# Optimization experiments

Measured on AMD Instinct MI355X. Metric: run time of the kernel, lower is better.

The kernel has to match this reference:

```python
import jax, jax.numpy as jnp
import numpy as np

N_NODES = 100000
N_EDGES = 3200000
N_FEAT = 512
N_GRAPHS = 64
N_EXTRA_LAYERS = 3  # layers 2..4, all 1->1


def setup_inputs() -> dict:
    key = jax.random.key(0)
    ks = jax.random.split(key, 10)
    x = jax.random.normal(ks[0], (N_NODES, N_FEAT), dtype=jnp.float32)
    edge_src = jax.random.randint(ks[1], (N_EDGES,), 0, N_NODES, dtype=jnp.int32)
    edge_dst = jax.random.randint(ks[2], (N_EDGES,), 0, N_NODES, dtype=jnp.int32)
    graph_ids = jnp.sort(jax.random.randint(ks[3], (N_NODES,), 0, N_GRAPHS, dtype=jnp.int32))
    W_neigh0 = jax.random.normal(ks[4], (N_FEAT, 1), dtype=jnp.float32) * 0.05
    W_self0 = jax.random.normal(ks[5], (N_FEAT, 1), dtype=jnp.float32) * 0.05
    b0 = jax.random.normal(ks[6], (1,), dtype=jnp.float32)
    W_neigh_r = jax.random.normal(ks[7], (N_EXTRA_LAYERS, 1, 1), dtype=jnp.float32)
    W_self_r = jax.random.normal(ks[8], (N_EXTRA_LAYERS, 1, 1), dtype=jnp.float32)
    b_r = jax.random.normal(ks[9], (N_EXTRA_LAYERS, 1), dtype=jnp.float32)
    return {"x": x, "edge_src": edge_src, "edge_dst": edge_dst, "graph_ids": graph_ids,
            "W_neigh0": W_neigh0, "W_self0": W_self0, "b0": b0,
            "W_neigh_r": W_neigh_r, "W_self_r": W_self_r, "b_r": b_r}


def _conv_wl(h, edge_src, edge_dst, W_neigh, W_self, b, n_nodes):
    # GraphConv(norm='none'): project first (in >= out here), gather at src, scatter-sum at dst, + bias
    proj = h @ W_neigh                      # [N, out]
    neigh = jax.ops.segment_sum(proj[edge_src], edge_dst, num_segments=n_nodes) + b
    return neigh + h @ W_self               # residual self-loop linear (no bias)


def reference(x, edge_src, edge_dst, graph_ids, W_neigh0, W_self0, b0, W_neigh_r, W_self_r, b_r):
    n = x.shape[0]
    xs = [x]
    h = jax.nn.relu(_conv_wl(x, edge_src, edge_dst, W_neigh0, W_self0, b0, n))
    xs.append(h)
    for i in range(W_neigh_r.shape[0]):
        h = jax.nn.relu(_conv_wl(h, edge_src, edge_dst, W_neigh_r[i], W_self_r[i], b_r[i], n))
        xs.append(h)
    hcat = jnp.concatenate(xs, axis=1)       # [N, F + num_layers] (concat_features=True)
    # dgl.sum_nodes: per-graph sum over the batched graph
    return jax.ops.segment_sum(hcat, graph_ids, num_segments=N_GRAPHS)  # [G, F + L]
```

## Files before the change

kernel.cpp:

```cpp
#include <hip/hip_runtime.h>

#define N_NODES  100000
#define N_EDGES  3200000
#define N_FEAT   512
#define N_GRAPHS 64
#define N_COLS   516
#define NBINS    1563
#define B1       256
#define EPB      (N_EDGES / B1)
#define CHUNK    25
#define NWAVES   (N_NODES / CHUNK)
#define SRC_MASK 0x1FFFF

__global__ __launch_bounds__(1024) void prep_kernel(
    const int* __restrict__ edst, const int* __restrict__ gid,
    int* __restrict__ histG, int* __restrict__ starts, float* __restrict__ outz)
{
    __shared__ int lh[NBINS];
    const int b = blockIdx.x, tid = threadIdx.x;
    const int gtid = b * 1024 + tid;

    if (gtid < N_GRAPHS * N_COLS) outz[gtid] = 0.f;
    if (gtid < N_NODES) {
        const int g = gid[gtid];
        const int gp = gtid ? gid[gtid - 1] : -1;
        for (int q = gp + 1; q <= g; ++q) starts[q] = gtid;
        if (gtid == N_NODES - 1)
            for (int q = g + 1; q <= N_GRAPHS; ++q) starts[q] = N_NODES;
    }
    for (int i = tid; i < NBINS; i += 1024) lh[i] = 0;
    __syncthreads();
    const int e0 = b * EPB;
    for (int e = e0 + tid; e < e0 + EPB; e += 1024)
        atomicAdd(&lh[edst[e] >> 6], 1);
    __syncthreads();
    for (int i = tid; i < NBINS; i += 1024) histG[i * B1 + b] = lh[i];
}

__device__ __forceinline__ void flush_cs(
    int si, int cur_g, const float a[8], int wave, int lane,
    float* __restrict__ pp, int* __restrict__ pt, float* __restrict__ out)
{
    if (si < 2) {
        const int slot = wave * 2 + si;
        if (lane == 0) pt[slot] = cur_g;
        float* d = pp + (size_t)slot * N_FEAT + lane * 8;
        *(float4*)d       = make_float4(a[0], a[1], a[2], a[3]);
        *(float4*)(d + 4) = make_float4(a[4], a[5], a[6], a[7]);
    } else {
        float* o = out + (size_t)cur_g * N_COLS + lane * 8;
        #pragma unroll
        for (int k = 0; k < 8; ++k) atomicAdd(o + k, a[k]);
    }
}

__global__ __launch_bounds__(256) void pass_x_kernel(
    const float* __restrict__ x, const int* __restrict__ gid,
    const float* __restrict__ wn, const float* __restrict__ ws,
    float* __restrict__ p0, float* __restrict__ s0,
    float* __restrict__ neigh, float* __restrict__ out,
    float* __restrict__ pp, int* __restrict__ pt)
{
    const int wave = (blockIdx.x * blockDim.x + threadIdx.x) >> 6;
    const int lane = threadIdx.x & 63;
    const int start = wave * CHUNK, end = start + CHUNK;

    for (int n = start + lane; n < end; n += 64) neigh[n] = 0.f;

    const float4 wna = *(const float4*)(wn + lane * 8);
    const float4 wnb = *(const float4*)(wn + lane * 8 + 4);
    const float4 wsa = *(const float4*)(ws + lane * 8);
    const float4 wsb = *(const float4*)(ws + lane * 8 + 4);

    float a[8] = {0.f, 0.f, 0.f, 0.f, 0.f, 0.f, 0.f, 0.f};
    int cur_g = gid[start];
    const bool uniform = (gid[end - 1] == cur_g);
    int si = 0;

    for (int n = start; n < end; ++n) {
        if (!uniform) {
            const int g = gid[n];
            if (g != cur_g) {
                flush_cs(si, cur_g, a, wave, lane, pp, pt, out);
                ++si;
                #pragma unroll
                for (int k = 0; k < 8; ++k) a[k] = 0.f;
                cur_g = g;
            }
        }
        const float* row = x + (size_t)n * N_FEAT;
        const float4 xa = *(const float4*)(row + lane * 8);
        const float4 xb = *(const float4*)(row + lane * 8 + 4);

        a[0] += xa.x; a[1] += xa.y; a[2] += xa.z; a[3] += xa.w;
        a[4] += xb.x; a[5] += xb.y; a[6] += xb.z; a[7] += xb.w;

        float dn = xa.x*wna.x + xa.y*wna.y + xa.z*wna.z + xa.w*wna.w
                 + xb.x*wnb.x + xb.y*wnb.y + xb.z*wnb.z + xb.w*wnb.w;
        float dv = xa.x*wsa.x + xa.y*wsa.y + xa.z*wsa.z + xa.w*wsa.w
                 + xb.x*wsb.x + xb.y*wsb.y + xb.z*wsb.z + xb.w*wsb.w;
        #pragma unroll
        for (int off = 32; off > 0; off >>= 1) {
            dn += __shfl_down(dn, off);
            dv += __shfl_down(dv, off);
        }
        if (lane == 0) { p0[n] = dn; s0[n] = dv; }
    }
    flush_cs(si, cur_g, a, wave, lane, pp, pt, out);
    ++si;
    if (lane == 0)
        for (int s2 = si; s2 < 2; ++s2) pt[wave * 2 + s2] = -1;
}

__global__ __launch_bounds__(512) void reduce_x_kernel(
    const float* __restrict__ pp, const int* __restrict__ pt,
    const int* __restrict__ starts, float* __restrict__ out)
{
    const int g = blockIdx.x, c = threadIdx.x;
    const int s = starts[g], e = starts[g + 1];
    float acc = 0.f;
    if (e > s) {
        const int w0 = s / CHUNK, w1 = (e - 1) / CHUNK;
        for (int w = w0; w <= w1; ++w) {
            #pragma unroll
            for (int k = 0; k < 2; ++k) {
                const int slot = w * 2 + k;
                if (pt[slot] == g) acc += pp[(size_t)slot * N_FEAT + c];
            }
        }
    }
    out[(size_t)g * N_COLS + c] += acc;
}

__global__ __launch_bounds__(256) void colscan_kernel(
    const int* __restrict__ histG, int* __restrict__ colscanG,
    int* __restrict__ totalG)
{
    __shared__ int sc[256];
    const int bin = blockIdx.x, t = threadIdx.x;
    const int v = histG[bin * B1 + t];
    sc[t] = v;
    __syncthreads();
    for (int off = 1; off < 256; off <<= 1) {
        const int a = (t >= off) ? sc[t - off] : 0;
        __syncthreads();
        sc[t] += a;
        __syncthreads();
    }
    colscanG[bin * B1 + t] = sc[t] - v;
    if (t == 255) totalG[bin] = sc[255];
}

__global__ __launch_bounds__(256) void scan2_kernel(
    const int* __restrict__ totalG, int* __restrict__ binstart)
{
    __shared__ int sc[256];
    const int t = threadIdx.x;
    const int CH = 7;
    int loc[CH];
    int s = 0;
    for (int i = 0; i < CH; ++i) {
        const int bin = t * CH + i;
        const int v = (bin < NBINS) ? totalG[bin] : 0;
        loc[i] = s; s += v;
    }
    const int my = s;
    sc[t] = my;
    __syncthreads();
    for (int off = 1; off < 256; off <<= 1) {
        const int a = (t >= off) ? sc[t - off] : 0;
        __syncthreads();
        sc[t] += a;
        __syncthreads();
    }
    const int texcl = sc[t] - my;
    for (int i = 0; i < CH; ++i) {
        const int bin = t * CH + i;
        if (bin < NBINS) binstart[bin] = texcl + loc[i];
    }
    if (t == 255) binstart[NBINS] = sc[255];
}

__global__ __launch_bounds__(1024) void reorder_kernel(
    const int* __restrict__ esrc, const int* __restrict__ edst,
    const int* __restrict__ binstart, const int* __restrict__ colscanG,
    int* __restrict__ sorted)
{
    __shared__ int offs[NBINS];
    const int b = blockIdx.x, tid = threadIdx.x;
    for (int i = tid; i < NBINS; i += 1024)
        offs[i] = binstart[i] + colscanG[i * B1 + b];
    __syncthreads();
    const int e0 = b * EPB;
    for (int e = e0 + tid; e < e0 + EPB; e += 1024) {
        const int s = esrc[e], d = edst[e];
        const int p = atomicAdd(&offs[d >> 6], 1);
        sorted[p] = s | ((d & 63) << 17);
    }
}

__global__ __launch_bounds__(256) void binned_scatter_kernel(
    const int* __restrict__ sorted, const int* __restrict__ binstart,
    const float* __restrict__ pin, const float* __restrict__ self_in,
    const float* __restrict__ wself_p, const float* __restrict__ bias_p,
    const float* __restrict__ wnext_p,
    float* __restrict__ h_out, float* __restrict__ p_next,
    const int* __restrict__ gid, float* __restrict__ out, int col)
{
    __shared__ float acc[4][64];
    const int b = blockIdx.x, tid = threadIdx.x;
    ((float*)acc)[tid] = 0.f;
    __syncthreads();

    const int st = binstart[b], en = binstart[b + 1];
    const int w = tid >> 6;
    for (int e = st + tid; e < en; e += 256) {
        const int v = sorted[e];
        atomicAdd(&acc[w][v >> 17], pin[v & SRC_MASK]);
    }
    __syncthreads();

    if (tid < 64) {
        const int n = b * 64 + tid;
        const bool valid = (n < N_NODES);
        float h = 0.f;
        int g = 0;
        if (valid) {
            const float nb = acc[0][tid] + acc[1][tid] + acc[2][tid] + acc[3][tid];
            const float sw = wself_p ? *wself_p : 1.0f;
            const float v = nb + *bias_p + sw * self_in[n];
            h = v > 0.f ? v : 0.f;
            h_out[n] = h;
            if (wnext_p) p_next[n] = h * (*wnext_p);
            g = gid[n];
        }
        const int g0 = __shfl(g, 0);
        if (__all(!valid || g == g0)) {
            float s = h;
            #pragma unroll
            for (int off = 32; off > 0; off >>= 1) s += __shfl_down(s, off);
            if (tid == 0) atomicAdd(&out[(size_t)g0 * N_COLS + col], s);
        } else if (valid) {
            atomicAdd(&out[(size_t)g * N_COLS + col], h);
        }
    }
}

extern "C" void kernel_launch(void* const* d_in, const int* in_sizes, int n_in,
                              void* d_out, int out_size, void* d_ws, size_t ws_size,
                              hipStream_t stream)
{
    (void)in_sizes; (void)n_in; (void)out_size; (void)ws_size;

    const float* x    = (const float*)d_in[0];
    const int*   esrc = (const int*)d_in[1];
    const int*   edst = (const int*)d_in[2];
    const int*   gid  = (const int*)d_in[3];
    const float* Wn0  = (const float*)d_in[4];
    const float* Ws0  = (const float*)d_in[5];
    const float* b0p  = (const float*)d_in[6];
    const float* Wnr  = (const float*)d_in[7];
    const float* Wsr  = (const float*)d_in[8];
    const float* brp  = (const float*)d_in[9];
    float* out = (float*)d_out;

    float* pp    = (float*)d_ws;
    float* bufP  = pp + (size_t)NWAVES * 2 * N_FEAT;
    float* bufP2 = bufP  + N_NODES;
    float* bufS  = bufP2 + N_NODES;
    float* bufH  = bufS  + N_NODES;
    int*   pt       = (int*)(bufH + N_NODES);
    int*   starts   = pt + NWAVES * 2;
    int*   binstart = starts + (N_GRAPHS + 1);
    int*   totalG   = binstart + NBINS + 1;
    int*   histG    = totalG + NBINS;
    int*   colscanG = histG + (size_t)NBINS * B1;
    int*   sorted   = colscanG + (size_t)NBINS * B1;

    prep_kernel<<<B1, 1024, 0, stream>>>(edst, gid, histG, starts, out);
    pass_x_kernel<<<NWAVES / 4, 256, 0, stream>>>(
        x, gid, Wn0, Ws0, bufP, bufS, bufP2 ,
        out, pp, pt);
    colscan_kernel<<<NBINS, 256, 0, stream>>>(histG, colscanG, totalG);
    scan2_kernel<<<1, 256, 0, stream>>>(totalG, binstart);
    reorder_kernel<<<B1, 1024, 0, stream>>>(esrc, edst, binstart, colscanG, sorted);
    reduce_x_kernel<<<N_GRAPHS, 512, 0, stream>>>(pp, pt, starts, out);

    binned_scatter_kernel<<<NBINS, 256, 0, stream>>>(
        sorted, binstart, bufP, bufS, nullptr, b0p, Wnr + 0, bufH, bufP2, gid, out, 512);
    binned_scatter_kernel<<<NBINS, 256, 0, stream>>>(
        sorted, binstart, bufP2, bufH, Wsr + 0, brp + 0, Wnr + 1, bufH, bufP, gid, out, 513);
    binned_scatter_kernel<<<NBINS, 256, 0, stream>>>(
        sorted, binstart, bufP, bufH, Wsr + 1, brp + 1, Wnr + 2, bufH, bufP2, gid, out, 514);
    binned_scatter_kernel<<<NBINS, 256, 0, stream>>>(
        sorted, binstart, bufP2, bufH, Wsr + 2, brp + 2, nullptr, bufH, nullptr, gid, out, 515);
}
```

Before: 509.8 us.

## Merge preprocessing and layer kernels into two cooperative grid-synced kernels

Replaces the ten separate kernel launches with two cooperative kernels. One handles histogram, column scan, the x pass, the bin prefix scan and the edge reorder, separated by grid.sync. The other runs the per-graph x reduction and all four scatter layers in a persistent 1024-block grid. The column scan now uses wave shuffles instead of a shared-memory block scan. This removes launch gaps between stages, but cooperative launches cap the grid at what can be co-resident, which limits parallelism, and grid.sync carries its own cost. The x pass now overlaps the column scan in one phase, and the x reduction overlaps the first layer.

```diff
diff --git a/kernel.cpp b/kernel.cpp
--- a/kernel.cpp
+++ b/kernel.cpp
@@ -1,4 +1,7 @@
 #include <hip/hip_runtime.h>
+#include <hip/hip_cooperative_groups.h>
+
+namespace cg = cooperative_groups;
 
 #define N_NODES  100000
 #define N_EDGES  3200000
@@ -11,31 +14,7 @@
 #define CHUNK    25
 #define NWAVES   (N_NODES / CHUNK)
 #define SRC_MASK 0x1FFFF
-
-__global__ __launch_bounds__(1024) void prep_kernel(
-    const int* __restrict__ edst, const int* __restrict__ gid,
-    int* __restrict__ histG, int* __restrict__ starts, float* __restrict__ outz)
-{
-    __shared__ int lh[NBINS];
-    const int b = blockIdx.x, tid = threadIdx.x;
-    const int gtid = b * 1024 + tid;
-
-    if (gtid < N_GRAPHS * N_COLS) outz[gtid] = 0.f;
-    if (gtid < N_NODES) {
-        const int g = gid[gtid];
-        const int gp = gtid ? gid[gtid - 1] : -1;
-        for (int q = gp + 1; q <= g; ++q) starts[q] = gtid;
-        if (gtid == N_NODES - 1)
-            for (int q = g + 1; q <= N_GRAPHS; ++q) starts[q] = N_NODES;
-    }
-    for (int i = tid; i < NBINS; i += 1024) lh[i] = 0;
-    __syncthreads();
-    const int e0 = b * EPB;
-    for (int e = e0 + tid; e < e0 + EPB; e += 1024)
-        atomicAdd(&lh[edst[e] >> 6], 1);
-    __syncthreads();
-    for (int i = tid; i < NBINS; i += 1024) histG[i * B1 + b] = lh[i];
-}
+#define GRID_B   1024
 
 __device__ __forceinline__ void flush_cs(
     int si, int cur_g, const float a[8], int wave, int lane,
@@ -54,196 +33,237 @@
     }
 }
 
-__global__ __launch_bounds__(256) void pass_x_kernel(
-    const float* __restrict__ x, const int* __restrict__ gid,
+__global__ __launch_bounds__(1024) void mega_prep_kernel(
+    const float* __restrict__ x, const int* __restrict__ esrc,
+    const int* __restrict__ edst, const int* __restrict__ gid,
     const float* __restrict__ wn, const float* __restrict__ ws,
     float* __restrict__ p0, float* __restrict__ s0,
-    float* __restrict__ neigh, float* __restrict__ out,
-    float* __restrict__ pp, int* __restrict__ pt)
-{
-    const int wave = (blockIdx.x * blockDim.x + threadIdx.x) >> 6;
-    const int lane = threadIdx.x & 63;
-    const int start = wave * CHUNK, end = start + CHUNK;
-
-    for (int n = start + lane; n < end; n += 64) neigh[n] = 0.f;
-
-    const float4 wna = *(const float4*)(wn + lane * 8);
-    const float4 wnb = *(const float4*)(wn + lane * 8 + 4);
-    const float4 wsa = *(const float4*)(ws + lane * 8);
-    const float4 wsb = *(const float4*)(ws + lane * 8 + 4);
-
-    float a[8] = {0.f, 0.f, 0.f, 0.f, 0.f, 0.f, 0.f, 0.f};
-    int cur_g = gid[start];
-    const bool uniform = (gid[end - 1] == cur_g);
-    int si = 0;
-
-    for (int n = start; n < end; ++n) {
-        if (!uniform) {
-            const int g = gid[n];
-            if (g != cur_g) {
-                flush_cs(si, cur_g, a, wave, lane, pp, pt, out);
-                ++si;
-                #pragma unroll
-                for (int k = 0; k < 8; ++k) a[k] = 0.f;
-                cur_g = g;
-            }
-        }
-        const float* row = x + (size_t)n * N_FEAT;
-        const float4 xa = *(const float4*)(row + lane * 8);
-        const float4 xb = *(const float4*)(row + lane * 8 + 4);
-
-        a[0] += xa.x; a[1] += xa.y; a[2] += xa.z; a[3] += xa.w;
-        a[4] += xb.x; a[5] += xb.y; a[6] += xb.z; a[7] += xb.w;
-
-        float dn = xa.x*wna.x + xa.y*wna.y + xa.z*wna.z + xa.w*wna.w
-                 + xb.x*wnb.x + xb.y*wnb.y + xb.z*wnb.z + xb.w*wnb.w;
-        float dv = xa.x*wsa.x + xa.y*wsa.y + xa.z*wsa.z + xa.w*wsa.w
-                 + xb.x*wsb.x + xb.y*wsb.y + xb.z*wsb.z + xb.w*wsb.w;
-        #pragma unroll
-        for (int off = 32; off > 0; off >>= 1) {
-            dn += __shfl_down(dn, off);
-            dv += __shfl_down(dv, off);
-        }
-        if (lane == 0) { p0[n] = dn; s0[n] = dv; }
-    }
-    flush_cs(si, cur_g, a, wave, lane, pp, pt, out);
-    ++si;
-    if (lane == 0)
-        for (int s2 = si; s2 < 2; ++s2) pt[wave * 2 + s2] = -1;
-}
-
-__global__ __launch_bounds__(512) void reduce_x_kernel(
-    const float* __restrict__ pp, const int* __restrict__ pt,
-    const int* __restrict__ starts, float* __restrict__ out)
-{
-    const int g = blockIdx.x, c = threadIdx.x;
-    const int s = starts[g], e = starts[g + 1];
-    float acc = 0.f;
-    if (e > s) {
-        const int w0 = s / CHUNK, w1 = (e - 1) / CHUNK;
-        for (int w = w0; w <= w1; ++w) {
+    float* __restrict__ out, float* __restrict__ pp, int* __restrict__ pt,
+    int* __restrict__ histG, int* __restrict__ colscanG, int* __restrict__ totalG,
+    int* __restrict__ starts, int* __restrict__ binstart, int* __restrict__ sorted)
+{
+    __shared__ int lh[NBINS];
+    cg::grid_group grid = cg::this_grid();
+    const int b = blockIdx.x, tid = threadIdx.x;
+    const int gtid = b * 1024 + tid;
+
+    if (gtid < N_GRAPHS * N_COLS) out[gtid] = 0.f;
+    if (gtid < N_NODES) {
+        const int g = gid[gtid];
+        const int gp = gtid ? gid[gtid - 1] : -1;
+        for (int q = gp + 1; q <= g; ++q) starts[q] = gtid;
+        if (gtid == N_NODES - 1)
+            for (int q = g + 1; q <= N_GRAPHS; ++q) starts[q] = N_NODES;
+    }
+    for (int i = tid; i < NBINS; i += 1024) lh[i] = 0;
+    __syncthreads();
+    {
+        const int e0 = b * EPB;
+        for (int e = e0 + tid; e < e0 + EPB; e += 1024)
+            atomicAdd(&lh[edst[e] >> 6], 1);
+    }
+    __syncthreads();
+    for (int i = tid; i < NBINS; i += 1024) histG[i * B1 + b] = lh[i];
+
+    grid.sync();
+
+    const int gwave = gtid >> 6;
+    const int lane = tid & 63;
+
+    if (gwave < NBINS) {
+        const int4 v = *(const int4*)(histG + (size_t)gwave * B1 + lane * 4);
+        const int s1 = v.x, s2 = s1 + v.y, s3 = s2 + v.z;
+        const int tot = s3 + v.w;
+        int incl = tot;
+        #pragma unroll
+        for (int off = 1; off < 64; off <<= 1) {
+            const int t = __shfl_up(incl, off);
+            if (lane >= off) incl += t;
+        }
+        const int excl = incl - tot;
+        *(int4*)(colscanG + (size_t)gwave * B1 + lane * 4) =
+            make_int4(excl, excl + s1, excl + s2, excl + s3);
+        if (lane == 63) totalG[gwave] = incl;
+    }
+
+    if (gwave < NWAVES) {
+        const int start = gwave * CHUNK, end = start + CHUNK;
+
+        const float4 wna = *(const float4*)(wn + lane * 8);
+        const float4 wnb = *(const float4*)(wn + lane * 8 + 4);
+        const float4 wsa = *(const float4*)(ws + lane * 8);
+        const float4 wsb = *(const float4*)(ws + lane * 8 + 4);
+
+        float a[8] = {0.f, 0.f, 0.f, 0.f, 0.f, 0.f, 0.f, 0.f};
+        int cur_g = gid[start];
+        const bool uniform = (gid[end - 1] == cur_g);
+        int si = 0;
+
+        for (int n = start; n < end; ++n) {
+            if (!uniform) {
+                const int g = gid[n];
+                if (g != cur_g) {
+                    flush_cs(si, cur_g, a, gwave, lane, pp, pt, out);
+                    ++si;
+                    #pragma unroll
+                    for (int k = 0; k < 8; ++k) a[k] = 0.f;
+                    cur_g = g;
+                }
+            }
+            const float* row = x + (size_t)n * N_FEAT;
+            const float4 xa = *(const float4*)(row + lane * 8);
+            const float4 xb = *(const float4*)(row + lane * 8 + 4);
+
+            a[0] += xa.x; a[1] += xa.y; a[2] += xa.z; a[3] += xa.w;
+            a[4] += xb.x; a[5] += xb.y; a[6] += xb.z; a[7] += xb.w;
+
+            float dn = xa.x*wna.x + xa.y*wna.y + xa.z*wna.z + xa.w*wna.w
+                     + xb.x*wnb.x + xb.y*wnb.y + xb.z*wnb.z + xb.w*wnb.w;
+            float dv = xa.x*wsa.x + xa.y*wsa.y + xa.z*wsa.z + xa.w*wsa.w
+                     + xb.x*wsb.x + xb.y*wsb.y + xb.z*wsb.z + xb.w*wsb.w;
             #pragma unroll
-            for (int k = 0; k < 2; ++k) {
-                const int slot = w * 2 + k;
-                if (pt[slot] == g) acc += pp[(size_t)slot * N_FEAT + c];
-            }
-        }
-    }
-    out[(size_t)g * N_COLS + c] += acc;
-}
-
-__global__ __launch_bounds__(256) void colscan_kernel(
-    const int* __restrict__ histG, int* __restrict__ colscanG,
-    int* __restrict__ totalG)
-{
-    __shared__ int sc[256];
-    const int bin = blockIdx.x, t = threadIdx.x;
-    const int v = histG[bin * B1 + t];
-    sc[t] = v;
+            for (int off = 32; off > 0; off >>= 1) {
+                dn += __shfl_down(dn, off);
+                dv += __shfl_down(dv, off);
+            }
+            if (lane == 0) { p0[n] = dn; s0[n] = dv; }
+        }
+        flush_cs(si, cur_g, a, gwave, lane, pp, pt, out);
+        ++si;
+        if (lane == 0)
+            for (int s2i = si; s2i < 2; ++s2i) pt[gwave * 2 + s2i] = -1;
+    }
+
+    grid.sync();
+
+    if (b == 0 && tid < 64) {
+        int loc[25];
+        int s = 0;
+        #pragma unroll
+        for (int i = 0; i < 25; ++i) {
+            const int bin = tid * 25 + i;
+            loc[i] = s;
+            s += (bin < NBINS) ? totalG[bin] : 0;
+        }
+        int incl = s;
+        #pragma unroll
+        for (int off = 1; off < 64; off <<= 1) {
+            const int t = __shfl_up(incl, off);
+            if (tid >= off) incl += t;
+        }
+        const int excl = incl - s;
+        #pragma unroll
+        for (int i = 0; i < 25; ++i) {
+            const int bin = tid * 25 + i;
+            if (bin <= NBINS) binstart[bin] = excl + loc[i];
+        }
+    }
+
+    grid.sync();
+
+    for (int i = tid; i < NBINS; i += 1024)
+        lh[i] = binstart[i] + colscanG[i * B1 + b];
     __syncthreads();
-    for (int off = 1; off < 256; off <<= 1) {
-        const int a = (t >= off) ? sc[t - off] : 0;
-        __syncthreads();
-        sc[t] += a;
-        __syncthreads();
-    }
-    colscanG[bin * B1 + t] = sc[t] - v;
-    if (t == 255) totalG[bin] = sc[255];
-}
-
-__global__ __launch_bounds__(256) void scan2_kernel(
-    const int* __restrict__ totalG, int* __restrict__ binstart)
-{
-    __shared__ int sc[256];
-    const int t = threadIdx.x;
-    const int CH = 7;
-    int loc[CH];
-    int s = 0;
-    for (int i = 0; i < CH; ++i) {
-        const int bin = t * CH + i;
-        const int v = (bin < NBINS) ? totalG[bin] : 0;
-        loc[i] = s; s += v;
-    }
-    const int my = s;
-    sc[t] = my;
-    __syncthreads();
-    for (int off = 1; off < 256; off <<= 1) {
-        const int a = (t >= off) ? sc[t - off] : 0;
-        __syncthreads();
-        sc[t] += a;
-        __syncthreads();
-    }
-    const int texcl = sc[t] - my;
-    for (int i = 0; i < CH; ++i) {
-        const int bin = t * CH + i;
-        if (bin < NBINS) binstart[bin] = texcl + loc[i];
-    }
-    if (t == 255) binstart[NBINS] = sc[255];
-}
-
-__global__ __launch_bounds__(1024) void reorder_kernel(
-    const int* __restrict__ esrc, const int* __restrict__ edst,
-    const int* __restrict__ binstart, const int* __restrict__ colscanG,
-    int* __restrict__ sorted)
-{
-    __shared__ int offs[NBINS];
-    const int b = blockIdx.x, tid = threadIdx.x;
-    for (int i = tid; i < NBINS; i += 1024)
-        offs[i] = binstart[i] + colscanG[i * B1 + b];
-    __syncthreads();
-    const int e0 = b * EPB;
-    for (int e = e0 + tid; e < e0 + EPB; e += 1024) {
-        const int s = esrc[e], d = edst[e];
-        const int p = atomicAdd(&offs[d >> 6], 1);
-        sorted[p] = s | ((d & 63) << 17);
-    }
-}
-
-__global__ __launch_bounds__(256) void binned_scatter_kernel(
+    {
+        const int e0 = b * EPB;
+        for (int e = e0 + tid; e < e0 + EPB; e += 1024) {
+            const int s = esrc[e], d = edst[e];
+            const int p = atomicAdd(&lh[d >> 6], 1);
+            sorted[p] = s | ((d & 63) << 17);
+        }
+    }
+}
+
+__device__ __forceinline__ void scatter_layer(
     const int* __restrict__ sorted, const int* __restrict__ binstart,
     const float* __restrict__ pin, const float* __restrict__ self_in,
     const float* __restrict__ wself_p, const float* __restrict__ bias_p,
     const float* __restrict__ wnext_p,
     float* __restrict__ h_out, float* __restrict__ p_next,
-    const int* __restrict__ gid, float* __restrict__ out, int col)
+    const int* __restrict__ gid, float* __restrict__ out, int col,
+    float (*acc)[64])
+{
+    const int tid = threadIdx.x;
+    const float sw    = wself_p ? *wself_p : 1.0f;
+    const float bias  = *bias_p;
+    const float wnext = wnext_p ? *wnext_p : 0.0f;
+
+    for (int b = blockIdx.x; b < NBINS; b += GRID_B) {
+        ((float*)acc)[tid] = 0.f;
+        __syncthreads();
+        const int st = binstart[b], en = binstart[b + 1];
+        const int w = tid >> 6;
+        for (int e = st + tid; e < en; e += 256) {
+            const int v = sorted[e];
+            atomicAdd(&acc[w][v >> 17], pin[v & SRC_MASK]);
+        }
+        __syncthreads();
+        if (tid < 64) {
+            const int n = b * 64 + tid;
+            const bool valid = (n < N_NODES);
+            float h = 0.f;
+            int g = 0;
+            if (valid) {
+                const float nb = acc[0][tid] + acc[1][tid] + acc[2][tid] + acc[3][tid];
+                const float v = nb + bias + sw * self_in[n];
+                h = v > 0.f ? v : 0.f;
+                h_out[n] = h;
+                if (wnext_p) p_next[n] = h * wnext;
+                g = gid[n];
+            }
+            const int g0 = __shfl(g, 0);
+            if (__all(!valid || g == g0)) {
+                float sacc = h;
+                #pragma unroll
+                for (int off = 32; off > 0; off >>= 1) sacc += __shfl_down(sacc, off);
+                if (tid == 0) atomicAdd(&out[(size_t)g0 * N_COLS + col], sacc);
+            } else if (valid) {
+                atomicAdd(&out[(size_t)g * N_COLS + col], h);
+            }
+        }
+        __syncthreads();
+    }
+}
+
+__global__ __launch_bounds__(256) void layers_kernel(
+    const int* __restrict__ sorted, const int* __restrict__ binstart,
+    const int* __restrict__ gid, float* __restrict__ out,
+    float* __restrict__ bufP, float* __restrict__ bufS,
+    float* __restrict__ bufP2, float* __restrict__ bufH,
+    const float* __restrict__ b0p, const float* __restrict__ Wnr,
+    const float* __restrict__ Wsr, const float* __restrict__ brp,
+    const float* __restrict__ pp, const int* __restrict__ pt,
+    const int* __restrict__ starts)
 {
     __shared__ float acc[4][64];
-    const int b = blockIdx.x, tid = threadIdx.x;
-    ((float*)acc)[tid] = 0.f;
-    __syncthreads();
-
-    const int st = binstart[b], en = binstart[b + 1];
-    const int w = tid >> 6;
-    for (int e = st + tid; e < en; e += 256) {
-        const int v = sorted[e];
-        atomicAdd(&acc[w][v >> 17], pin[v & SRC_MASK]);
-    }
-    __syncthreads();
-
-    if (tid < 64) {
-        const int n = b * 64 + tid;
-        const bool valid = (n < N_NODES);
-        float h = 0.f;
-        int g = 0;
-        if (valid) {
-            const float nb = acc[0][tid] + acc[1][tid] + acc[2][tid] + acc[3][tid];
-            const float sw = wself_p ? *wself_p : 1.0f;
-            const float v = nb + *bias_p + sw * self_in[n];
-            h = v > 0.f ? v : 0.f;
-            h_out[n] = h;
-            if (wnext_p) p_next[n] = h * (*wnext_p);
-            g = gid[n];
-        }
-        const int g0 = __shfl(g, 0);
-        if (__all(!valid || g == g0)) {
-            float s = h;
-            #pragma unroll
-            for (int off = 32; off > 0; off >>= 1) s += __shfl_down(s, off);
-            if (tid == 0) atomicAdd(&out[(size_t)g0 * N_COLS + col], s);
-        } else if (valid) {
-            atomicAdd(&out[(size_t)g * N_COLS + col], h);
-        }
-    }
+    cg::grid_group grid = cg::this_grid();
+
+    if (blockIdx.x >= GRID_B - N_GRAPHS) {
+        const int g = blockIdx.x - (GRID_B - N_GRAPHS);
+        const int s = starts[g], e = starts[g + 1];
+        for (int c = threadIdx.x; c < N_FEAT; c += 256) {
+            float accv = 0.f;
+            if (e > s) {
+                const int w0 = s / CHUNK, w1 = (e - 1) / CHUNK;
+                for (int w = w0; w <= w1; ++w) {
+                    #pragma unroll
+                    for (int k = 0; k < 2; ++k) {
+                        const int slot = w * 2 + k;
+                        if (pt[slot] == g) accv += pp[(size_t)slot * N_FEAT + c];
+                    }
+                }
+            }
+            out[(size_t)g * N_COLS + c] += accv;
+        }
+    }
+
+    scatter_layer(sorted, binstart, bufP,  bufS, nullptr, b0p,     Wnr + 0, bufH, bufP2, gid, out, 512, acc);
+    grid.sync();
+    scatter_layer(sorted, binstart, bufP2, bufH, Wsr + 0, brp + 0, Wnr + 1, bufH, bufP,  gid, out, 513, acc);
+    grid.sync();
+    scatter_layer(sorted, binstart, bufP,  bufH, Wsr + 1, brp + 1, Wnr + 2, bufH, bufP2, gid, out, 514, acc);
+    grid.sync();
+    scatter_layer(sorted, binstart, bufP2, bufH, Wsr + 2, brp + 2, nullptr, bufH, nullptr, gid, out, 515, acc);
 }
 
 extern "C" void kernel_launch(void* const* d_in, const int* in_sizes, int n_in,
@@ -271,27 +291,31 @@
     float* bufH  = bufS  + N_NODES;
     int*   pt       = (int*)(bufH + N_NODES);
     int*   starts   = pt + NWAVES * 2;
-    int*   binstart = starts + (N_GRAPHS + 1);
-    int*   totalG   = binstart + NBINS + 1;
-    int*   histG    = totalG + NBINS;
+    int*   binstart = starts + 68;
+    int*   totalG   = binstart + 1564;
+    int*   histG    = totalG + 1564;
     int*   colscanG = histG + (size_t)NBINS * B1;
     int*   sorted   = colscanG + (size_t)NBINS * B1;
 
-    prep_kernel<<<B1, 1024, 0, stream>>>(edst, gid, histG, starts, out);
-    pass_x_kernel<<<NWAVES / 4, 256, 0, stream>>>(
-        x, gid, Wn0, Ws0, bufP, bufS, bufP2 ,
-        out, pp, pt);
-    colscan_kernel<<<NBINS, 256, 0, stream>>>(histG, colscanG, totalG);
-    scan2_kernel<<<1, 256, 0, stream>>>(totalG, binstart);
-    reorder_kernel<<<B1, 1024, 0, stream>>>(esrc, edst, binstart, colscanG, sorted);
-    reduce_x_kernel<<<N_GRAPHS, 512, 0, stream>>>(pp, pt, starts, out);
-
-    binned_scatter_kernel<<<NBINS, 256, 0, stream>>>(
-        sorted, binstart, bufP, bufS, nullptr, b0p, Wnr + 0, bufH, bufP2, gid, out, 512);
-    binned_scatter_kernel<<<NBINS, 256, 0, stream>>>(
-        sorted, binstart, bufP2, bufH, Wsr + 0, brp + 0, Wnr + 1, bufH, bufP, gid, out, 513);
-    binned_scatter_kernel<<<NBINS, 256, 0, stream>>>(
-        sorted, binstart, bufP, bufH, Wsr + 1, brp + 1, Wnr + 2, bufH, bufP2, gid, out, 514);
-    binned_scatter_kernel<<<NBINS, 256, 0, stream>>>(
-        sorted, binstart, bufP2, bufH, Wsr + 2, brp + 2, nullptr, bufH, nullptr, gid, out, 515);
-}
+    {
+        void* args[] = {
+            (void*)&x, (void*)&esrc, (void*)&edst, (void*)&gid,
+            (void*)&Wn0, (void*)&Ws0, (void*)&bufP, (void*)&bufS,
+            (void*)&out, (void*)&pp, (void*)&pt,
+            (void*)&histG, (void*)&colscanG, (void*)&totalG,
+            (void*)&starts, (void*)&binstart, (void*)&sorted
+        };
+        hipLaunchCooperativeKernel((const void*)mega_prep_kernel,
+                                   dim3(B1), dim3(1024), args, 0, stream);
+    }
+    {
+        void* args[] = {
+            (void*)&sorted, (void*)&binstart, (void*)&gid, (void*)&out,
+            (void*)&bufP, (void*)&bufS, (void*)&bufP2, (void*)&bufH,
+            (void*)&b0p, (void*)&Wnr, (void*)&Wsr, (void*)&brp,
+            (void*)&pp, (void*)&pt, (void*)&starts
+        };
+        hipLaunchCooperativeKernel((const void*)layers_kernel,
+                                   dim3(GRID_B), dim3(256), args, 0, stream);
+    }
+}
```

After: 1.022 ms. 101% more time.

## Bin edges by source and push-scatter with global atomics instead of pull-gather

Applied to the files above, without the earlier changes.

Edges are now binned by source node rather than destination. Each block computes the previous layer's activation for its 64 source nodes into shared memory, then atomically adds into a global per-layer neighbour buffer indexed by destination, and a new final kernel finishes the last layer. This swaps random global gathers of the projection for random global float atomics. It also adds four zeroed neighbour buffers and one extra kernel launch.

```diff
diff --git a/kernel.cpp b/kernel.cpp
--- a/kernel.cpp
+++ b/kernel.cpp
@@ -6,21 +6,24 @@
 #define N_GRAPHS 64
 #define N_COLS   516
 #define NBINS    1563
+#define NEIGH_PAD 100032
 #define B1       256
 #define EPB      (N_EDGES / B1)
 #define CHUNK    25
 #define NWAVES   (N_NODES / CHUNK)
-#define SRC_MASK 0x1FFFF
+#define DST_MASK 0x1FFFF
 
 __global__ __launch_bounds__(1024) void prep_kernel(
-    const int* __restrict__ edst, const int* __restrict__ gid,
-    int* __restrict__ histG, int* __restrict__ starts, float* __restrict__ outz)
+    const int* __restrict__ esrc, const int* __restrict__ gid,
+    int* __restrict__ histG, int* __restrict__ starts,
+    float* __restrict__ outz, float* __restrict__ neigh)
 {
     __shared__ int lh[NBINS];
     const int b = blockIdx.x, tid = threadIdx.x;
     const int gtid = b * 1024 + tid;
 
     if (gtid < N_GRAPHS * N_COLS) outz[gtid] = 0.f;
+    for (int i = gtid; i < 4 * NEIGH_PAD; i += B1 * 1024) neigh[i] = 0.f;
     if (gtid < N_NODES) {
         const int g = gid[gtid];
         const int gp = gtid ? gid[gtid - 1] : -1;
@@ -32,7 +35,7 @@
     __syncthreads();
     const int e0 = b * EPB;
     for (int e = e0 + tid; e < e0 + EPB; e += 1024)
-        atomicAdd(&lh[edst[e] >> 6], 1);
+        atomicAdd(&lh[esrc[e] >> 6], 1);
     __syncthreads();
     for (int i = tid; i < NBINS; i += 1024) histG[i * B1 + b] = lh[i];
 }
@@ -58,14 +61,12 @@
     const float* __restrict__ x, const int* __restrict__ gid,
     const float* __restrict__ wn, const float* __restrict__ ws,
     float* __restrict__ p0, float* __restrict__ s0,
-    float* __restrict__ neigh, float* __restrict__ out,
+    float* __restrict__ out,
     float* __restrict__ pp, int* __restrict__ pt)
 {
     const int wave = (blockIdx.x * blockDim.x + threadIdx.x) >> 6;
     const int lane = threadIdx.x & 63;
     const int start = wave * CHUNK, end = start + CHUNK;
-
-    for (int n = start + lane; n < end; n += 64) neigh[n] = 0.f;
 
     const float4 wna = *(const float4*)(wn + lane * 8);
     const float4 wnb = *(const float4*)(wn + lane * 8 + 4);
@@ -194,55 +195,87 @@
     const int e0 = b * EPB;
     for (int e = e0 + tid; e < e0 + EPB; e += 1024) {
         const int s = esrc[e], d = edst[e];
-        const int p = atomicAdd(&offs[d >> 6], 1);
-        sorted[p] = s | ((d & 63) << 17);
-    }
-}
-
-__global__ __launch_bounds__(256) void binned_scatter_kernel(
+        const int p = atomicAdd(&offs[s >> 6], 1);
+        sorted[p] = d | ((s & 63) << 17);
+    }
+}
+
+__global__ __launch_bounds__(256) void scatter_kernel(
     const int* __restrict__ sorted, const int* __restrict__ binstart,
-    const float* __restrict__ pin, const float* __restrict__ self_in,
-    const float* __restrict__ wself_p, const float* __restrict__ bias_p,
+    const float* __restrict__ neigh_in,
+    const float* __restrict__ p_in,
+    const float* __restrict__ self_in,
+    const float* __restrict__ wself_p,
+    const float* __restrict__ bias_p,
     const float* __restrict__ wnext_p,
-    float* __restrict__ h_out, float* __restrict__ p_next,
-    const int* __restrict__ gid, float* __restrict__ out, int col)
-{
-    __shared__ float acc[4][64];
+    float* __restrict__ h_out,
+    const int* __restrict__ gid, float* __restrict__ out, int col,
+    float* __restrict__ neigh_out)
+{
+    __shared__ float ps[64];
     const int b = blockIdx.x, tid = threadIdx.x;
-    ((float*)acc)[tid] = 0.f;
-    __syncthreads();
-
-    const int st = binstart[b], en = binstart[b + 1];
-    const int w = tid >> 6;
-    for (int e = st + tid; e < en; e += 256) {
-        const int v = sorted[e];
-        atomicAdd(&acc[w][v >> 17], pin[v & SRC_MASK]);
-    }
-    __syncthreads();
 
     if (tid < 64) {
         const int n = b * 64 + tid;
         const bool valid = (n < N_NODES);
-        float h = 0.f;
-        int g = 0;
-        if (valid) {
-            const float nb = acc[0][tid] + acc[1][tid] + acc[2][tid] + acc[3][tid];
-            const float sw = wself_p ? *wself_p : 1.0f;
-            const float v = nb + *bias_p + sw * self_in[n];
-            h = v > 0.f ? v : 0.f;
-            h_out[n] = h;
-            if (wnext_p) p_next[n] = h * (*wnext_p);
-            g = gid[n];
+        float p = 0.f;
+        if (neigh_in) {
+            float h = 0.f;
+            int g = 0;
+            if (valid) {
+                const float sw = wself_p ? *wself_p : 1.0f;
+                const float v = neigh_in[n] + *bias_p + sw * self_in[n];
+                h = v > 0.f ? v : 0.f;
+                h_out[n] = h;
+                g = gid[n];
+            }
+            p = h * (*wnext_p);
+            const int g0 = __shfl(g, 0);
+            if (__all(!valid || g == g0)) {
+                float s = h;
+                #pragma unroll
+                for (int off = 32; off > 0; off >>= 1) s += __shfl_down(s, off);
+                if (tid == 0) atomicAdd(&out[(size_t)g0 * N_COLS + col], s);
+            } else if (valid) {
+                atomicAdd(&out[(size_t)g * N_COLS + col], h);
+            }
+        } else {
+            if (valid) p = p_in[n];
         }
-        const int g0 = __shfl(g, 0);
-        if (__all(!valid || g == g0)) {
-            float s = h;
-            #pragma unroll
-            for (int off = 32; off > 0; off >>= 1) s += __shfl_down(s, off);
-            if (tid == 0) atomicAdd(&out[(size_t)g0 * N_COLS + col], s);
-        } else if (valid) {
-            atomicAdd(&out[(size_t)g * N_COLS + col], h);
-        }
+        ps[tid] = p;
+    }
+    __syncthreads();
+
+    const int st = binstart[b], en = binstart[b + 1];
+    for (int e = st + tid; e < en; e += 256) {
+        const int v = sorted[e];
+        atomicAdd(&neigh_out[v & DST_MASK], ps[v >> 17]);
+    }
+}
+
+__global__ __launch_bounds__(64) void final_kernel(
+    const float* __restrict__ neigh_in, const float* __restrict__ h_prev,
+    const float* __restrict__ wself_p, const float* __restrict__ bias_p,
+    const int* __restrict__ gid, float* __restrict__ out)
+{
+    const int b = blockIdx.x, tid = threadIdx.x;
+    const int n = b * 64 + tid;
+    const bool valid = (n < N_NODES);
+    float h = 0.f;
+    int g = 0;
+    if (valid) {
+        const float v = neigh_in[n] + *bias_p + (*wself_p) * h_prev[n];
+        h = v > 0.f ? v : 0.f;
+        g = gid[n];
+    }
+    const int g0 = __shfl(g, 0);
+    if (__all(!valid || g == g0)) {
+        float s = h;
+        #pragma unroll
+        for (int off = 32; off > 0; off >>= 1) s += __shfl_down(s, off);
+        if (tid == 0) atomicAdd(&out[(size_t)g0 * N_COLS + 515], s);
+    } else if (valid) {
+        atomicAdd(&out[(size_t)g * N_COLS + 515], h);
     }
 }
 
@@ -266,32 +299,40 @@
 
     float* pp    = (float*)d_ws;
     float* bufP  = pp + (size_t)NWAVES * 2 * N_FEAT;
-    float* bufP2 = bufP  + N_NODES;
-    float* bufS  = bufP2 + N_NODES;
-    float* bufH  = bufS  + N_NODES;
-    int*   pt       = (int*)(bufH + N_NODES);
+    float* bufS  = bufP + N_NODES;
+    float* bufH1 = bufS + N_NODES;
+    float* bufH2 = bufH1 + N_NODES;
+    float* bufH3 = bufH2 + N_NODES;
+    float* neigh = bufH3 + N_NODES;
+    float* n0 = neigh,             *n1 = neigh + NEIGH_PAD;
+    float* n2 = neigh + 2*NEIGH_PAD, *n3 = neigh + 3*NEIGH_PAD;
+    int*   pt       = (int*)(neigh + 4 * NEIGH_PAD);
     int*   starts   = pt + NWAVES * 2;
-    int*   binstart = starts + (N_GRAPHS + 1);
-    int*   totalG   = binstart + NBINS + 1;
-    int*   histG    = totalG + NBINS;
+    int*   binstart = starts + 68;
+    int*   totalG   = binstart + 1564;
+    int*   histG    = totalG + 1564;
     int*   colscanG = histG + (size_t)NBINS * B1;
     int*   sorted   = colscanG + (size_t)NBINS * B1;
 
-    prep_kernel<<<B1, 1024, 0, stream>>>(edst, gid, histG, starts, out);
+    prep_kernel<<<B1, 1024, 0, stream>>>(esrc, gid, histG, starts, out, neigh);
     pass_x_kernel<<<NWAVES / 4, 256, 0, stream>>>(
-        x, gid, Wn0, Ws0, bufP, bufS, bufP2 ,
-        out, pp, pt);
+        x, gid, Wn0, Ws0, bufP, bufS, out, pp, pt);
     colscan_kernel<<<NBINS, 256, 0, stream>>>(histG, colscanG, totalG);
     scan2_kernel<<<1, 256, 0, stream>>>(totalG, binstart);
     reorder_kernel<<<B1, 1024, 0, stream>>>(esrc, edst, binstart, colscanG, sorted);
     reduce_x_kernel<<<N_GRAPHS, 512, 0, stream>>>(pp, pt, starts, out);
 
-    binned_scatter_kernel<<<NBINS, 256, 0, stream>>>(
-        sorted, binstart, bufP, bufS, nullptr, b0p, Wnr + 0, bufH, bufP2, gid, out, 512);
-    binned_scatter_kernel<<<NBINS, 256, 0, stream>>>(
-        sorted, binstart, bufP2, bufH, Wsr + 0, brp + 0, Wnr + 1, bufH, bufP, gid, out, 513);
-    binned_scatter_kernel<<<NBINS, 256, 0, stream>>>(
-        sorted, binstart, bufP, bufH, Wsr + 1, brp + 1, Wnr + 2, bufH, bufP2, gid, out, 514);
-    binned_scatter_kernel<<<NBINS, 256, 0, stream>>>(
-        sorted, binstart, bufP2, bufH, Wsr + 2, brp + 2, nullptr, bufH, nullptr, gid, out, 515);
-}
+    scatter_kernel<<<NBINS, 256, 0, stream>>>(
+        sorted, binstart, nullptr, bufP, nullptr, nullptr, nullptr, nullptr,
+        nullptr, gid, out, -1, n0);
+    scatter_kernel<<<NBINS, 256, 0, stream>>>(
+        sorted, binstart, n0, nullptr, bufS, nullptr, b0p, Wnr + 0,
+        bufH1, gid, out, 512, n1);
+    scatter_kernel<<<NBINS, 256, 0, stream>>>(
+        sorted, binstart, n1, nullptr, bufH1, Wsr + 0, brp + 0, Wnr + 1,
+        bufH2, gid, out, 513, n2);
+    scatter_kernel<<<NBINS, 256, 0, stream>>>(
+        sorted, binstart, n2, nullptr, bufH2, Wsr + 1, brp + 1, Wnr + 2,
+        bufH3, gid, out, 514, n3);
+    final_kernel<<<NBINS, 64, 0, stream>>>(n3, bufH3, Wsr + 2, brp + 2, gid, out);
+}
```

After: 1.087 ms. 113% more time.

## Bin edges into 2D src/dst tiles so source values come from LDS

Applied to the files above, without the earlier changes.

Edges are now bucketed by (source chunk of 4096, destination chunk of 8192) instead of by destination only. Each tile block stages its source projections and a destination accumulator in shared memory, so the random gathers move from global memory to LDS. Per-source-chunk partials go to a global buffer, and a new reduce/update kernel sums the 25 partials per node. This adds a partial-buffer round trip and one extra kernel launch per layer. The prep histogram is also replicated eight ways to cut shared-atomic contention.

```diff
diff --git a/kernel.cpp b/kernel.cpp
--- a/kernel.cpp
+++ b/kernel.cpp
@@ -5,18 +5,26 @@
 #define N_FEAT   512
 #define N_GRAPHS 64
 #define N_COLS   516
-#define NBINS    1563
 #define B1       256
 #define EPB      (N_EDGES / B1)
 #define CHUNK    25
 #define NWAVES   (N_NODES / CHUNK)
-#define SRC_MASK 0x1FFFF
+
+#define SC_SHIFT 12
+#define SC       4096
+#define DC_SHIFT 13
+#define DC       8192
+#define NS       25
+#define ND       13
+#define NT       (NS * ND)
+#define NPAD     (ND * DC)
 
 __global__ __launch_bounds__(1024) void prep_kernel(
-    const int* __restrict__ edst, const int* __restrict__ gid,
+    const int* __restrict__ esrc, const int* __restrict__ edst,
+    const int* __restrict__ gid,
     int* __restrict__ histG, int* __restrict__ starts, float* __restrict__ outz)
 {
-    __shared__ int lh[NBINS];
+    __shared__ int lh[8][NT];
     const int b = blockIdx.x, tid = threadIdx.x;
     const int gtid = b * 1024 + tid;
 
@@ -28,13 +36,21 @@
         if (gtid == N_NODES - 1)
             for (int q = g + 1; q <= N_GRAPHS; ++q) starts[q] = N_NODES;
     }
-    for (int i = tid; i < NBINS; i += 1024) lh[i] = 0;
-    __syncthreads();
+    for (int i = tid; i < 8 * NT; i += 1024) ((int*)lh)[i] = 0;
+    __syncthreads();
+    const int r = (tid >> 7) & 7;
     const int e0 = b * EPB;
-    for (int e = e0 + tid; e < e0 + EPB; e += 1024)
-        atomicAdd(&lh[edst[e] >> 6], 1);
-    __syncthreads();
-    for (int i = tid; i < NBINS; i += 1024) histG[i * B1 + b] = lh[i];
+    for (int e = e0 + tid; e < e0 + EPB; e += 1024) {
+        const int t = (esrc[e] >> SC_SHIFT) * ND + (edst[e] >> DC_SHIFT);
+        atomicAdd(&lh[r][t], 1);
+    }
+    __syncthreads();
+    for (int i = tid; i < NT; i += 1024) {
+        int s = 0;
+        s += lh[0][i]; s += lh[1][i]; s += lh[2][i]; s += lh[3][i];
+        s += lh[4][i]; s += lh[5][i]; s += lh[6][i]; s += lh[7][i];
+        histG[i * B1 + b] = s;
+    }
 }
 
 __device__ __forceinline__ void flush_cs(
@@ -58,14 +74,12 @@
     const float* __restrict__ x, const int* __restrict__ gid,
     const float* __restrict__ wn, const float* __restrict__ ws,
     float* __restrict__ p0, float* __restrict__ s0,
-    float* __restrict__ neigh, float* __restrict__ out,
+    float* __restrict__ out,
     float* __restrict__ pp, int* __restrict__ pt)
 {
     const int wave = (blockIdx.x * blockDim.x + threadIdx.x) >> 6;
     const int lane = threadIdx.x & 63;
     const int start = wave * CHUNK, end = start + CHUNK;
-
-    for (int n = start + lane; n < end; n += 64) neigh[n] = 0.f;
 
     const float4 wna = *(const float4*)(wn + lane * 8);
     const float4 wnb = *(const float4*)(wn + lane * 8 + 4);
@@ -156,13 +170,14 @@
 {
     __shared__ int sc[256];
     const int t = threadIdx.x;
-    const int CH = 7;
-    int loc[CH];
+    int loc0, loc1;
     int s = 0;
-    for (int i = 0; i < CH; ++i) {
-        const int bin = t * CH + i;
-        const int v = (bin < NBINS) ? totalG[bin] : 0;
-        loc[i] = s; s += v;
+    {
+        const int bin = t * 2;
+        const int v0 = (bin < NT) ? totalG[bin] : 0;
+        loc0 = s; s += v0;
+        const int v1 = (bin + 1 < NT) ? totalG[bin + 1] : 0;
+        loc1 = s; s += v1;
     }
     const int my = s;
     sc[t] = my;
@@ -174,11 +189,9 @@
         __syncthreads();
     }
     const int texcl = sc[t] - my;
-    for (int i = 0; i < CH; ++i) {
-        const int bin = t * CH + i;
-        if (bin < NBINS) binstart[bin] = texcl + loc[i];
-    }
-    if (t == 255) binstart[NBINS] = sc[255];
+    if (t * 2 < NT)     binstart[t * 2]     = texcl + loc0;
+    if (t * 2 + 1 < NT) binstart[t * 2 + 1] = texcl + loc1;
+    if (t == 255) binstart[NT] = sc[255];
 }
 
 __global__ __launch_bounds__(1024) void reorder_kernel(
@@ -186,63 +199,79 @@
     const int* __restrict__ binstart, const int* __restrict__ colscanG,
     int* __restrict__ sorted)
 {
-    __shared__ int offs[NBINS];
+    __shared__ int offs[NT];
     const int b = blockIdx.x, tid = threadIdx.x;
-    for (int i = tid; i < NBINS; i += 1024)
+    for (int i = tid; i < NT; i += 1024)
         offs[i] = binstart[i] + colscanG[i * B1 + b];
     __syncthreads();
     const int e0 = b * EPB;
     for (int e = e0 + tid; e < e0 + EPB; e += 1024) {
         const int s = esrc[e], d = edst[e];
-        const int p = atomicAdd(&offs[d >> 6], 1);
-        sorted[p] = s | ((d & 63) << 17);
-    }
-}
-
-__global__ __launch_bounds__(256) void binned_scatter_kernel(
-    const int* __restrict__ sorted, const int* __restrict__ binstart,
-    const float* __restrict__ pin, const float* __restrict__ self_in,
-    const float* __restrict__ wself_p, const float* __restrict__ bias_p,
+        const int t = (s >> SC_SHIFT) * ND + (d >> DC_SHIFT);
+        const int p = atomicAdd(&offs[t], 1);
+        sorted[p] = ((s & (SC - 1)) << DC_SHIFT) | (d & (DC - 1));
+    }
+}
+
+__global__ __launch_bounds__(1024) void tile_scatter_kernel(
+    const int* __restrict__ sorted, const int* __restrict__ tilestart,
+    const float* __restrict__ ps_global, float* __restrict__ partial)
+{
+    __shared__ float ps[SC];
+    __shared__ float acc[DC];
+    const int t = blockIdx.x, tid = threadIdx.x;
+    const int s = t / ND, d = t - s * ND;
+
+    const int nbase = s << SC_SHIFT;
+    for (int i = tid; i < SC; i += 1024) {
+        const int n = nbase + i;
+        ps[i] = (n < N_NODES) ? ps_global[n] : 0.f;
+    }
+    for (int i = tid; i < DC; i += 1024) acc[i] = 0.f;
+    __syncthreads();
+
+    const int st = tilestart[t], en = tilestart[t + 1];
+    for (int e = st + tid; e < en; e += 1024) {
+        const int v = sorted[e];
+        atomicAdd(&acc[v & (DC - 1)], ps[v >> DC_SHIFT]);
+    }
+    __syncthreads();
+
+    float* dst = partial + (size_t)s * NPAD + ((size_t)d << DC_SHIFT);
+    for (int i = tid; i < DC; i += 1024) dst[i] = acc[i];
+}
+
+__global__ __launch_bounds__(256) void reduce_update_kernel(
+    const float* __restrict__ partial, const float* __restrict__ self_in,
+    const float* __restrict__ wself_p,
+    const float* __restrict__ bias_p,
     const float* __restrict__ wnext_p,
     float* __restrict__ h_out, float* __restrict__ p_next,
     const int* __restrict__ gid, float* __restrict__ out, int col)
 {
-    __shared__ float acc[4][64];
-    const int b = blockIdx.x, tid = threadIdx.x;
-    ((float*)acc)[tid] = 0.f;
-    __syncthreads();
-
-    const int st = binstart[b], en = binstart[b + 1];
-    const int w = tid >> 6;
-    for (int e = st + tid; e < en; e += 256) {
-        const int v = sorted[e];
-        atomicAdd(&acc[w][v >> 17], pin[v & SRC_MASK]);
-    }
-    __syncthreads();
-
-    if (tid < 64) {
-        const int n = b * 64 + tid;
-        const bool valid = (n < N_NODES);
-        float h = 0.f;
-        int g = 0;
-        if (valid) {
-            const float nb = acc[0][tid] + acc[1][tid] + acc[2][tid] + acc[3][tid];
-            const float sw = wself_p ? *wself_p : 1.0f;
-            const float v = nb + *bias_p + sw * self_in[n];
-            h = v > 0.f ? v : 0.f;
-            h_out[n] = h;
-            if (wnext_p) p_next[n] = h * (*wnext_p);
-            g = gid[n];
-        }
-        const int g0 = __shfl(g, 0);
-        if (__all(!valid || g == g0)) {
-            float s = h;
-            #pragma unroll
-            for (int off = 32; off > 0; off >>= 1) s += __shfl_down(s, off);
-            if (tid == 0) atomicAdd(&out[(size_t)g0 * N_COLS + col], s);
-        } else if (valid) {
-            atomicAdd(&out[(size_t)g * N_COLS + col], h);
-        }
+    const int n = blockIdx.x * 256 + threadIdx.x;
+    const bool valid = (n < N_NODES);
+    float h = 0.f;
+    int g = 0;
+    if (valid) {
+        float nb = 0.f;
+        #pragma unroll
+        for (int s = 0; s < NS; ++s) nb += partial[(size_t)s * NPAD + n];
+        const float sw = wself_p ? *wself_p : 1.0f;
+        const float v = nb + *bias_p + sw * self_in[n];
+        h = v > 0.f ? v : 0.f;
+        h_out[n] = h;
+        if (wnext_p) p_next[n] = h * (*wnext_p);
+        g = gid[n];
+    }
+    const int g0 = __shfl(g, 0);
+    if (__all(!valid || g == g0)) {
+        float sv = h;
+        #pragma unroll
+        for (int off = 32; off > 0; off >>= 1) sv += __shfl_down(sv, off);
+        if ((threadIdx.x & 63) == 0) atomicAdd(&out[(size_t)g0 * N_COLS + col], sv);
+    } else if (valid) {
+        atomicAdd(&out[(size_t)g * N_COLS + col], h);
     }
 }
 
@@ -264,34 +293,41 @@
     const float* brp  = (const float*)d_in[9];
     float* out = (float*)d_out;
 
-    float* pp    = (float*)d_ws;
-    float* bufP  = pp + (size_t)NWAVES * 2 * N_FEAT;
-    float* bufP2 = bufP  + N_NODES;
-    float* bufS  = bufP2 + N_NODES;
-    float* bufH  = bufS  + N_NODES;
-    int*   pt       = (int*)(bufH + N_NODES);
+    float* pp      = (float*)d_ws;
+    float* bufP    = pp + (size_t)NWAVES * 2 * N_FEAT;
+    float* bufS    = bufP + N_NODES;
+    float* bufH1   = bufS + N_NODES;
+    float* bufH2   = bufH1 + N_NODES;
+    float* bufPn   = bufH2 + N_NODES;
+    float* partial = bufPn + N_NODES;
+    int*   pt       = (int*)(partial + (size_t)NS * NPAD);
     int*   starts   = pt + NWAVES * 2;
-    int*   binstart = starts + (N_GRAPHS + 1);
-    int*   totalG   = binstart + NBINS + 1;
-    int*   histG    = totalG + NBINS;
-    int*   colscanG = histG + (size_t)NBINS * B1;
-    int*   sorted   = colscanG + (size_t)NBINS * B1;
-
-    prep_kernel<<<B1, 1024, 0, stream>>>(edst, gid, histG, starts, out);
+    int*   binstart = starts + 68;
+    int*   totalG   = binstart + 328;
+    int*   histG    = totalG + 328;
+    int*   colscanG = histG + (size_t)NT * B1;
+    int*   sorted   = colscanG + (size_t)NT * B1;
+
+    prep_kernel<<<B1, 1024, 0, stream>>>(esrc, edst, gid, histG, starts, out);
     pass_x_kernel<<<NWAVES / 4, 256, 0, stream>>>(
-        x, gid, Wn0, Ws0, bufP, bufS, bufP2 ,
-        out, pp, pt);
-    colscan_kernel<<<NBINS, 256, 0, stream>>>(histG, colscanG, totalG);
+        x, gid, Wn0, Ws0, bufP, bufS, out, pp, pt);
+    colscan_kernel<<<NT, 256, 0, stream>>>(histG, colscanG, totalG);
     scan2_kernel<<<1, 256, 0, stream>>>(totalG, binstart);
     reorder_kernel<<<B1, 1024, 0, stream>>>(esrc, edst, binstart, colscanG, sorted);
     reduce_x_kernel<<<N_GRAPHS, 512, 0, stream>>>(pp, pt, starts, out);
 
-    binned_scatter_kernel<<<NBINS, 256, 0, stream>>>(
-        sorted, binstart, bufP, bufS, nullptr, b0p, Wnr + 0, bufH, bufP2, gid, out, 512);
-    binned_scatter_kernel<<<NBINS, 256, 0, stream>>>(
-        sorted, binstart, bufP2, bufH, Wsr + 0, brp + 0, Wnr + 1, bufH, bufP, gid, out, 513);
-    binned_scatter_kernel<<<NBINS, 256, 0, stream>>>(
-        sorted, binstart, bufP, bufH, Wsr + 1, brp + 1, Wnr + 2, bufH, bufP2, gid, out, 514);
-    binned_scatter_kernel<<<NBINS, 256, 0, stream>>>(
-        sorted, binstart, bufP2, bufH, Wsr + 2, brp + 2, nullptr, bufH, nullptr, gid, out, 515);
-}
+    const int RB = (N_NODES + 255) / 256;
+
+    tile_scatter_kernel<<<NT, 1024, 0, stream>>>(sorted, binstart, bufP, partial);
+    reduce_update_kernel<<<RB, 256, 0, stream>>>(
+        partial, bufS, nullptr, b0p, Wnr + 0, bufH1, bufPn, gid, out, 512);
+    tile_scatter_kernel<<<NT, 1024, 0, stream>>>(sorted, binstart, bufPn, partial);
+    reduce_update_kernel<<<RB, 256, 0, stream>>>(
+        partial, bufH1, Wsr + 0, brp + 0, Wnr + 1, bufH2, bufPn, gid, out, 513);
+    tile_scatter_kernel<<<NT, 1024, 0, stream>>>(sorted, binstart, bufPn, partial);
+    reduce_update_kernel<<<RB, 256, 0, stream>>>(
+        partial, bufH2, Wsr + 1, brp + 1, Wnr + 2, bufH1, bufPn, gid, out, 514);
+    tile_scatter_kernel<<<NT, 1024, 0, stream>>>(sorted, binstart, bufPn, partial);
+    reduce_update_kernel<<<RB, 256, 0, stream>>>(
+        partial, bufH1, Wsr + 2, brp + 2, nullptr, bufH2, nullptr, gid, out, 515);
+}
```

Result: slower. 546.6 us (+7.2%).
